# Optimization experiments

Measured on AMD Instinct MI355X. Metric: run time of the kernel, lower is better.

Reference implementation:

```python
import jax, jax.numpy as jnp
import numpy as np

B, T, IN, H, NH = 64, 512, 1024, 1024, 4
HD = H // NH  # head_dim = 256
NG = 3        # gates: z (update), r (reset), n (candidate)


def setup_inputs() -> dict:
    key = jax.random.key(0)
    k1, k2, k3, k4, k5 = jax.random.split(key, 5)
    inp = jax.random.normal(k1, (B, T, IN), dtype=jnp.float32)
    # nn.Linear(input_size, 3*hidden_size): weight [3H, IN], bias [3H]
    W = jax.random.normal(k2, (IN, NG * H), dtype=jnp.float32) / np.sqrt(IN)
    bW = jax.random.normal(k3, (NG * H,), dtype=jnp.float32) * 0.02
    # recurrent R: [num_heads, head_dim_in, num_gates, head_dim_out], std=1/sqrt(head_dim)
    R = jax.random.normal(k4, (NH, HD, NG, HD), dtype=jnp.float32) / np.sqrt(HD)
    b = jax.random.normal(k5, (NH, NG, HD), dtype=jnp.float32)
    return {"input": inp, "W": W, "bW": bW, "R": R, "b": b}


def _gru_scan(Wx, R, b, h0):
    # Wx: [T, B, NH, NG, HD], h0: [B, NH, HD]
    def step(h, wx):
        # recurrent gate preactivations: Ry[b,h,g,o] = sum_i h[b,h,i] R[h,i,g,o]
        ry = jnp.einsum('bhi,higo->bhgo', h, R)
        z = jax.nn.sigmoid(wx[:, :, 0] + ry[:, :, 0] + b[:, 0])
        r = jax.nn.sigmoid(wx[:, :, 1] + ry[:, :, 1] + b[:, 1])
        n = jnp.tanh(wx[:, :, 2] + r * ry[:, :, 2] + b[:, 2])
        h_new = z * h + (1.0 - z) * n
        return h_new, h_new

    h_last, hs = jax.lax.scan(step, h0, Wx)
    return hs, h_last  # hs: [T, B, NH, HD]


def reference(input, W, bW, R, b):
    bs, sl = input.shape[0], input.shape[1]
    # input projection for all timesteps at once
    Wx = input @ W + bW                               # [B, T, NG*H]
    Wx = Wx.reshape(bs, sl, NG, NH, HD)
    Wx = jnp.transpose(Wx, (1, 0, 3, 2, 4))           # [T, B, NH, NG, HD]
    h0 = jnp.zeros((bs, NH, HD), dtype=input.dtype)
    hs, h_last = _gru_scan(Wx, R, b, h0)
    h = jnp.transpose(hs, (1, 0, 2, 3)).reshape(bs, sl, H)   # [B, T, H]
    hn = h_last.reshape(1, bs, H)                             # [num_layers=1, B, H]
    return h, hn
```

## Files before the change

kernel.cpp:

```cpp
#include <hip/hip_runtime.h>
#include <hip/hip_fp16.h>


typedef _Float16 f16x8 __attribute__((ext_vector_type(8)));
typedef _Float16 f16x2 __attribute__((ext_vector_type(2)));
typedef float    f32x4 __attribute__((ext_vector_type(4)));

#define AS1 __attribute__((address_space(1)))
#define AS3 __attribute__((address_space(3)))

__device__ __forceinline__ void async_ld16(const void* g, void* l) {
    __builtin_amdgcn_global_load_lds((const AS1 void*)g, (AS3 void*)l, 16, 0, 0);
}

__device__ __forceinline__ float sigmoidf_(float x) {
    return 1.f / (1.f + __expf(-x));
}
__device__ __forceinline__ float tanhf_(float x) {
    float e = __expf(-2.f * fabsf(x));
    float r = (1.f - e) / (1.f + e);
    return copysignf(r, x);
}

__device__ __forceinline__ float dot2f(f16x2 a, f16x2 b, float c) {
    asm("v_dot2_f32_f16 %0, %1, %2, %0" : "+v"(c) : "v"(a), "v"(b));
    return c;
}

__global__ __launch_bounds__(256) void cast_to_f16(const float* __restrict__ in,
                                                   _Float16* __restrict__ out, int n8) {
    int i = blockIdx.x * 256 + threadIdx.x;
    if (i >= n8) return;
    const float4* p = (const float4*)in;
    float4 a = p[2 * i], b = p[2 * i + 1];
    f16x8 r;
    r[0] = (_Float16)a.x; r[1] = (_Float16)a.y; r[2] = (_Float16)a.z; r[3] = (_Float16)a.w;
    r[4] = (_Float16)b.x; r[5] = (_Float16)b.y; r[6] = (_Float16)b.z; r[7] = (_Float16)b.w;
    *(f16x8*)(out + (size_t)i * 8) = r;
}

__global__ __launch_bounds__(256) void transpose_cast(const float* __restrict__ W,
                                                      _Float16* __restrict__ WT) {
    __shared__ float tile[32][33];
    const int tx = threadIdx.x, ty = threadIdx.y;
    const int n0 = blockIdx.x * 32, k0 = blockIdx.y * 32;
#pragma unroll
    for (int j = 0; j < 32; j += 8)
        tile[ty + j][tx] = W[(size_t)(k0 + ty + j) * 3072 + n0 + tx];
    __syncthreads();
#pragma unroll
    for (int j = 0; j < 32; j += 8)
        WT[(size_t)(n0 + ty + j) * 1024 + k0 + tx] = (_Float16)tile[tx][ty + j];
}

__global__ __launch_bounds__(256) void gemm_wx(const _Float16* __restrict__ A,
                                               const _Float16* __restrict__ BT,
                                               const float* __restrict__ bW,
                                               const float* __restrict__ bR,
                                               float* __restrict__ Wx) {
    __shared__ _Float16 As[128 * 32];
    __shared__ _Float16 Bs[128 * 32];
    const int tid  = threadIdx.x;
    const int wave = tid >> 6, lane = tid & 63;
    const int m0 = blockIdx.y * 128, n0 = blockIdx.x * 128;
    const int wm = (wave >> 1) * 64, wn = (wave & 1) * 64;
    const int r16 = lane & 15, kq = lane >> 4;

    f32x4 acc[4][4];
#pragma unroll
    for (int m = 0; m < 4; m++)
#pragma unroll
        for (int n = 0; n < 4; n++) acc[m][n] = (f32x4){0.f, 0.f, 0.f, 0.f};

    const int srow = wave * 32 + (lane >> 2);
    const int scol = (lane & 3) * 8;

    for (int kt = 0; kt < 32; kt++) {
        const int k0 = kt * 32;
#pragma unroll
        for (int j = 0; j < 2; j++) {
            async_ld16(A  + (size_t)(m0 + srow + j * 16) * 1024 + k0 + scol,
                       As + (wave * 32 + j * 16) * 32);
            async_ld16(BT + (size_t)(n0 + srow + j * 16) * 1024 + k0 + scol,
                       Bs + (wave * 32 + j * 16) * 32);
        }
        __syncthreads();
        f16x8 af[4], bf[4];
#pragma unroll
        for (int m = 0; m < 4; m++) af[m] = *(const f16x8*)(As + (wm + m * 16 + r16) * 32 + kq * 8);
#pragma unroll
        for (int n = 0; n < 4; n++) bf[n] = *(const f16x8*)(Bs + (wn + n * 16 + r16) * 32 + kq * 8);
#pragma unroll
        for (int m = 0; m < 4; m++)
#pragma unroll
            for (int n = 0; n < 4; n++)
                acc[m][n] = __builtin_amdgcn_mfma_f32_16x16x32_f16(af[m], bf[n], acc[m][n], 0, 0, 0);
        __syncthreads();
    }

#pragma unroll
    for (int m = 0; m < 4; m++) {
        const int row0 = m0 + wm + m * 16 + (lane >> 4) * 4;
#pragma unroll
        for (int n = 0; n < 4; n++) {
            const int col  = n0 + wn + n * 16 + r16;
            const int g    = col >> 10, head = (col >> 8) & 3, o = col & 255;
            const float bias = bW[col] + bR[head * 768 + g * 256 + o];
#pragma unroll
            for (int q = 0; q < 4; q++) {
                const int rr = row0 + q;
                const int t = rr & 511, bb = rr >> 9;
                Wx[(((size_t)t * 64 + bb) * 12 + head * 3 + g) * 256 + o] = acc[m][n][q] + bias;
            }
        }
    }
}

__global__ __launch_bounds__(1024, 4) void scan_persist(const float* __restrict__ R,
                                                        const float* __restrict__ Wx,
                                                        float* __restrict__ out) {
    const int head = blockIdx.x >> 6;
    const int b    = blockIdx.x & 63;
    const int t    = threadIdx.x;
    const int o    = t & 255;
    const int ih   = t >> 8;

    __shared__ _Float16 h16[256];
    __shared__ float red[4][3][256];

    f16x2 Rr[3][32];
    {
        const float* Rb = R + (((size_t)head * 256 + ih * 64) * 3) * 256 + o;
#pragma unroll
        for (int i2 = 0; i2 < 32; i2++) {
#pragma unroll
            for (int g = 0; g < 3; g++) {
                const float lo = Rb[((size_t)(2 * i2) * 3 + g) * 256];
                const float hi = Rb[((size_t)(2 * i2 + 1) * 3 + g) * 256];
                f16x2 p; p[0] = (_Float16)lo; p[1] = (_Float16)hi;
                Rr[g][i2] = p;
            }
        }
    }

    float hreg = 0.f;
    float wxc0 = 0.f, wxc1 = 0.f, wxc2 = 0.f;
    if (t < 256) {
        const float* p = Wx + ((size_t)b * 12 + head * 3) * 256 + o;
        wxc0 = p[0]; wxc1 = p[256]; wxc2 = p[512];
        h16[o] = (_Float16)0.f;
    }
    __syncthreads();

    float* outp = out + (size_t)b * 512 * 1024 + head * 256 + o;

    for (int step = 0; step < 512; step++) {
        float wxn0 = 0.f, wxn1 = 0.f, wxn2 = 0.f;
        if (t < 256 && step < 511) {
            const float* p = Wx + (((size_t)(step + 1) * 64 + b) * 12 + head * 3) * 256 + o;
            wxn0 = p[0]; wxn1 = p[256]; wxn2 = p[512];
        }
        float az = 0.f, ar = 0.f, an = 0.f;
        const f16x8* hp = (const f16x8*)(h16 + ih * 64);
#pragma unroll
        for (int k = 0; k < 8; k++) {
            union { f16x8 v; f16x2 p[4]; } u;
            u.v = hp[k];
#pragma unroll
            for (int j = 0; j < 4; j++) {
                az = dot2f(Rr[0][k * 4 + j], u.p[j], az);
                ar = dot2f(Rr[1][k * 4 + j], u.p[j], ar);
                an = dot2f(Rr[2][k * 4 + j], u.p[j], an);
            }
        }
        red[ih][0][o] = az; red[ih][1][o] = ar; red[ih][2][o] = an;
        __syncthreads();
        if (t < 256) {
            const float z  = sigmoidf_(wxc0 + red[0][0][o] + red[1][0][o] + red[2][0][o] + red[3][0][o]);
            const float r  = sigmoidf_(wxc1 + red[0][1][o] + red[1][1][o] + red[2][1][o] + red[3][1][o]);
            const float n  = tanhf_(wxc2 + r * (red[0][2][o] + red[1][2][o] + red[2][2][o] + red[3][2][o]));
            const float hn = z * hreg + (1.f - z) * n;
            hreg = hn;
            outp[(size_t)step * 1024] = hn;
            h16[o] = (_Float16)hn;
        }
        wxc0 = wxn0; wxc1 = wxn1; wxc2 = wxn2;
        __syncthreads();
    }
}

__global__ __launch_bounds__(256) void copy_hn(float* __restrict__ out) {
    const int idx = blockIdx.x * 256 + threadIdx.x;
    out[(size_t)64 * 512 * 1024 + idx] =
        out[((size_t)(idx >> 10) * 512 + 511) * 1024 + (idx & 1023)];
}

extern "C" void kernel_launch(void* const* d_in, const int* in_sizes, int n_in,
                              void* d_out, int out_size, void* d_ws, size_t ws_size,
                              hipStream_t stream) {
    (void)in_sizes; (void)n_in; (void)out_size; (void)ws_size;
    const float* inp = (const float*)d_in[0];
    const float* W   = (const float*)d_in[1];
    const float* bW  = (const float*)d_in[2];
    const float* R   = (const float*)d_in[3];
    const float* bR  = (const float*)d_in[4];
    float* out = (float*)d_out;

    _Float16* A16 = (_Float16*)d_ws;
    _Float16* WT  = (_Float16*)((char*)d_ws + 67108864);
    float*    Wx  = (float*)((char*)d_ws + 73400320);

    cast_to_f16<<<16384, 256, 0, stream>>>(inp, A16, 4194304);
    transpose_cast<<<dim3(96, 32), dim3(32, 8), 0, stream>>>(W, WT);
    gemm_wx<<<dim3(24, 256), 256, 0, stream>>>(A16, WT, bW, bR, Wx);
    scan_persist<<<256, 1024, 0, stream>>>(R, Wx, out);
    copy_hn<<<256, 256, 0, stream>>>(out);
}
```

Baseline: 1.059 ms.

## Reduce GRU scan partials with lane swizzles and double-buffer the hidden state

In the scan kernel, threads are remapped so the four k-slices of one output unit sit in adjacent lanes. Their dot-product partials are then summed with two ds_swizzle butterfly steps instead of a shared-memory reduction array, which removes one __syncthreads and the LDS traffic in every one of the 512 sequential steps. The hidden state is double-buffered in padded shared memory, so reads and writes within a step do not race and one barrier per step is enough. The dot2 asm is also replaced by the compiler builtin where it is available. In exchange, the one-time R loads become less coalesced, and gate math now runs on one lane in four spread across all waves.

```diff
diff --git a/kernel.cpp b/kernel.cpp
--- a/kernel.cpp
+++ b/kernel.cpp
@@ -22,10 +22,16 @@
     return copysignf(r, x);
 }
 
+#if defined(__has_builtin) && __has_builtin(__builtin_amdgcn_fdot2)
+__device__ __forceinline__ float dot2f(f16x2 a, f16x2 b, float c) {
+    return __builtin_amdgcn_fdot2(a, b, c, false);
+}
+#else
 __device__ __forceinline__ float dot2f(f16x2 a, f16x2 b, float c) {
     asm("v_dot2_f32_f16 %0, %1, %2, %0" : "+v"(c) : "v"(a), "v"(b));
     return c;
 }
+#endif
 
 __global__ __launch_bounds__(256) void cast_to_f16(const float* __restrict__ in,
                                                    _Float16* __restrict__ out, int n8) {
@@ -122,11 +128,10 @@
     const int head = blockIdx.x >> 6;
     const int b    = blockIdx.x & 63;
     const int t    = threadIdx.x;
-    const int o    = t & 255;
-    const int ih   = t >> 8;
-
-    __shared__ _Float16 h16[256];
-    __shared__ float red[4][3][256];
+    const int o    = t >> 2;
+    const int ih   = t & 3;
+
+    __shared__ _Float16 h_s[2 * 4 * 72];
 
     f16x2 Rr[3][32];
     {
@@ -143,12 +148,13 @@
         }
     }
 
+    for (int p = t; p < 2 * 4 * 72; p += 1024) h_s[p] = (_Float16)0.f;
+
     float hreg = 0.f;
     float wxc0 = 0.f, wxc1 = 0.f, wxc2 = 0.f;
-    if (t < 256) {
+    if (ih == 0) {
         const float* p = Wx + ((size_t)b * 12 + head * 3) * 256 + o;
         wxc0 = p[0]; wxc1 = p[256]; wxc2 = p[512];
-        h16[o] = (_Float16)0.f;
     }
     __syncthreads();
 
@@ -156,12 +162,12 @@
 
     for (int step = 0; step < 512; step++) {
         float wxn0 = 0.f, wxn1 = 0.f, wxn2 = 0.f;
-        if (t < 256 && step < 511) {
+        if (ih == 0 && step < 511) {
             const float* p = Wx + (((size_t)(step + 1) * 64 + b) * 12 + head * 3) * 256 + o;
             wxn0 = p[0]; wxn1 = p[256]; wxn2 = p[512];
         }
         float az = 0.f, ar = 0.f, an = 0.f;
-        const f16x8* hp = (const f16x8*)(h16 + ih * 64);
+        const f16x8* hp = (const f16x8*)(h_s + (step & 1) * 288 + ih * 72);
 #pragma unroll
         for (int k = 0; k < 8; k++) {
             union { f16x8 v; f16x2 p[4]; } u;
@@ -173,16 +179,21 @@
                 an = dot2f(Rr[2][k * 4 + j], u.p[j], an);
             }
         }
-        red[ih][0][o] = az; red[ih][1][o] = ar; red[ih][2][o] = an;
-        __syncthreads();
-        if (t < 256) {
-            const float z  = sigmoidf_(wxc0 + red[0][0][o] + red[1][0][o] + red[2][0][o] + red[3][0][o]);
-            const float r  = sigmoidf_(wxc1 + red[0][1][o] + red[1][1][o] + red[2][1][o] + red[3][1][o]);
-            const float n  = tanhf_(wxc2 + r * (red[0][2][o] + red[1][2][o] + red[2][2][o] + red[3][2][o]));
+        az += __int_as_float(__builtin_amdgcn_ds_swizzle(__float_as_int(az), 0x041F));
+        ar += __int_as_float(__builtin_amdgcn_ds_swizzle(__float_as_int(ar), 0x041F));
+        an += __int_as_float(__builtin_amdgcn_ds_swizzle(__float_as_int(an), 0x041F));
+        az += __int_as_float(__builtin_amdgcn_ds_swizzle(__float_as_int(az), 0x081F));
+        ar += __int_as_float(__builtin_amdgcn_ds_swizzle(__float_as_int(ar), 0x081F));
+        an += __int_as_float(__builtin_amdgcn_ds_swizzle(__float_as_int(an), 0x081F));
+
+        if (ih == 0) {
+            const float z  = sigmoidf_(wxc0 + az);
+            const float r  = sigmoidf_(wxc1 + ar);
+            const float n  = tanhf_(wxc2 + r * an);
             const float hn = z * hreg + (1.f - z) * n;
             hreg = hn;
             outp[(size_t)step * 1024] = hn;
-            h16[o] = (_Float16)hn;
+            h_s[((step + 1) & 1) * 288 + (o >> 6) * 72 + (o & 63)] = (_Float16)hn;
         }
         wxc0 = wxn0; wxc1 = wxn1; wxc2 = wxn2;
         __syncthreads();
```

Result: slower. 1.246 ms (+17.7%).

## Batch GRU scan over 16 sequences per block using MFMA with register/LDS-resident R

Applied to the files above, without the earlier changes.

Replaces the per-(head,batch) dot2 scan, which used 256 blocks of 1024 threads, with an MFMA-based scan. Each of 16 blocks handles one head and 16 batch rows, so the recurrent matmul runs on matrix cores. Most of R is kept in registers and the remaining quarter in LDS. Wx is now stored in fp16, and a new repack kernel lays it out per block and timestep for vectorized loads. The trade-off is far fewer blocks on the serial critical path, extra fp16 rounding of the gate inputs, and an additional repack pass.

```diff
diff --git a/kernel.cpp b/kernel.cpp
--- a/kernel.cpp
+++ b/kernel.cpp
@@ -3,7 +3,7 @@
 
 
 typedef _Float16 f16x8 __attribute__((ext_vector_type(8)));
-typedef _Float16 f16x2 __attribute__((ext_vector_type(2)));
+typedef _Float16 f16x4 __attribute__((ext_vector_type(4)));
 typedef float    f32x4 __attribute__((ext_vector_type(4)));
 
 #define AS1 __attribute__((address_space(1)))
@@ -20,11 +20,6 @@
     float e = __expf(-2.f * fabsf(x));
     float r = (1.f - e) / (1.f + e);
     return copysignf(r, x);
-}
-
-__device__ __forceinline__ float dot2f(f16x2 a, f16x2 b, float c) {
-    asm("v_dot2_f32_f16 %0, %1, %2, %0" : "+v"(c) : "v"(a), "v"(b));
-    return c;
 }
 
 __global__ __launch_bounds__(256) void cast_to_f16(const float* __restrict__ in,
@@ -57,7 +52,7 @@
                                                const _Float16* __restrict__ BT,
                                                const float* __restrict__ bW,
                                                const float* __restrict__ bR,
-                                               float* __restrict__ Wx) {
+                                               _Float16* __restrict__ WxA) {
     __shared__ _Float16 As[128 * 32];
     __shared__ _Float16 Bs[128 * 32];
     const int tid  = threadIdx.x;
@@ -110,82 +105,150 @@
             for (int q = 0; q < 4; q++) {
                 const int rr = row0 + q;
                 const int t = rr & 511, bb = rr >> 9;
-                Wx[(((size_t)t * 64 + bb) * 12 + head * 3 + g) * 256 + o] = acc[m][n][q] + bias;
+                WxA[(((size_t)t * 64 + bb) * 12 + head * 3 + g) * 256 + o] =
+                    (_Float16)(acc[m][n][q] + bias);
             }
         }
     }
 }
 
-__global__ __launch_bounds__(1024, 4) void scan_persist(const float* __restrict__ R,
-                                                        const float* __restrict__ Wx,
-                                                        float* __restrict__ out) {
-    const int head = blockIdx.x >> 6;
-    const int b    = blockIdx.x & 63;
-    const int t    = threadIdx.x;
-    const int o    = t & 255;
-    const int ih   = t >> 8;
-
-    __shared__ _Float16 h16[256];
-    __shared__ float red[4][3][256];
-
-    f16x2 Rr[3][32];
+__global__ __launch_bounds__(256) void repack_wx(const _Float16* __restrict__ src,
+                                                 _Float16* __restrict__ dst) {
+    __shared__ _Float16 tile[16 * 768];
+    const int bx = blockIdx.x;
+    const int t = bx >> 4, head = (bx >> 2) & 3, bg = bx & 3;
+    const int tid = threadIdx.x;
     {
-        const float* Rb = R + (((size_t)head * 256 + ih * 64) * 3) * 256 + o;
-#pragma unroll
-        for (int i2 = 0; i2 < 32; i2++) {
-#pragma unroll
-            for (int g = 0; g < 3; g++) {
-                const float lo = Rb[((size_t)(2 * i2) * 3 + g) * 256];
-                const float hi = Rb[((size_t)(2 * i2 + 1) * 3 + g) * 256];
-                f16x2 p; p[0] = (_Float16)lo; p[1] = (_Float16)hi;
-                Rr[g][i2] = p;
+        const int b = tid >> 4, seg = tid & 15;
+        const _Float16* sp = src + (((size_t)t * 64 + bg * 16 + b) * 12 + head * 3) * 256 + seg * 48;
+        _Float16* tp = tile + b * 768 + seg * 48;
+#pragma unroll
+        for (int u = 0; u < 6; u++)
+            *(float4*)(tp + u * 8) = *(const float4*)(sp + u * 8);
+    }
+    __syncthreads();
+    {
+        const int o = tid;
+        _Float16 buf[48];
+#pragma unroll
+        for (int g = 0; g < 3; g++)
+#pragma unroll
+            for (int b = 0; b < 16; b++)
+                buf[g * 16 + b] = tile[b * 768 + g * 256 + o];
+        _Float16* dp = dst + (size_t)bx * 12288 + o * 48;
+#pragma unroll
+        for (int u = 0; u < 6; u++)
+            *(float4*)(dp + u * 8) = *(const float4*)(buf + u * 8);
+    }
+}
+
+__global__ __launch_bounds__(256) void scan_mfma(const float* __restrict__ R,
+                                                 const _Float16* __restrict__ Wxb,
+                                                 float* __restrict__ out) {
+    extern __shared__ char smem[];
+    _Float16* h16 = (_Float16*)smem;
+    _Float16* Rst = (_Float16*)(smem + 17024);
+
+    const int bx = blockIdx.x;
+    const int head = bx >> 2, bg = bx & 3;
+    const int tid = threadIdx.x;
+    const int w = tid >> 6, l = tid & 63;
+    const int c = l & 15, rq = l >> 4;
+
+    for (int idx = tid; idx < 3 * 64 * 256; idx += 256) {
+        const int g = idx >> 14, i = (idx >> 8) & 63, o = idx & 255;
+        Rst[((size_t)g * 256 + o) * 74 + i] =
+            (_Float16)R[(((size_t)head * 256 + 192 + i) * 3 + g) * 256 + o];
+    }
+    for (int idx = tid; idx < 2 * 16 * 266; idx += 256) h16[idx] = (_Float16)0.f;
+
+    f16x8 Bf[12][6];
+#pragma unroll
+    for (int osi = 0; osi < 4; osi++)
+#pragma unroll
+        for (int g = 0; g < 3; g++) {
+            const int o = (osi * 4 + w) * 16 + c;
+            const float* rp = R + ((size_t)head * 256 * 3 + g) * 256 + o;
+#pragma unroll
+            for (int kt = 0; kt < 6; kt++) {
+                f16x8 v;
+#pragma unroll
+                for (int j = 0; j < 8; j++)
+                    v[j] = (_Float16)rp[(size_t)(kt * 32 + rq * 8 + j) * 768];
+                Bf[osi * 3 + g][kt] = v;
             }
         }
-    }
-
-    float hreg = 0.f;
-    float wxc0 = 0.f, wxc1 = 0.f, wxc2 = 0.f;
-    if (t < 256) {
-        const float* p = Wx + ((size_t)b * 12 + head * 3) * 256 + o;
-        wxc0 = p[0]; wxc1 = p[256]; wxc2 = p[512];
-        h16[o] = (_Float16)0.f;
+
+    float hprev[4][4];
+#pragma unroll
+    for (int osi = 0; osi < 4; osi++)
+#pragma unroll
+        for (int q = 0; q < 4; q++) hprev[osi][q] = 0.f;
+
+    f16x4 wx[12];
+    {
+        const _Float16* wp = Wxb + (size_t)bx * 12288;
+#pragma unroll
+        for (int osi = 0; osi < 4; osi++)
+#pragma unroll
+            for (int g = 0; g < 3; g++)
+                wx[osi * 3 + g] = *(const f16x4*)(wp + (((osi * 4 + w) * 16 + c) * 3 + g) * 16 + rq * 4);
     }
     __syncthreads();
 
-    float* outp = out + (size_t)b * 512 * 1024 + head * 256 + o;
-
-    for (int step = 0; step < 512; step++) {
-        float wxn0 = 0.f, wxn1 = 0.f, wxn2 = 0.f;
-        if (t < 256 && step < 511) {
-            const float* p = Wx + (((size_t)(step + 1) * 64 + b) * 12 + head * 3) * 256 + o;
-            wxn0 = p[0]; wxn1 = p[256]; wxn2 = p[512];
-        }
-        float az = 0.f, ar = 0.f, an = 0.f;
-        const f16x8* hp = (const f16x8*)(h16 + ih * 64);
-#pragma unroll
-        for (int k = 0; k < 8; k++) {
-            union { f16x8 v; f16x2 p[4]; } u;
-            u.v = hp[k];
-#pragma unroll
-            for (int j = 0; j < 4; j++) {
-                az = dot2f(Rr[0][k * 4 + j], u.p[j], az);
-                ar = dot2f(Rr[1][k * 4 + j], u.p[j], ar);
-                an = dot2f(Rr[2][k * 4 + j], u.p[j], an);
+    int cur = 0;
+    for (int t = 0; t < 512; t++) {
+        const _Float16* hc = h16 + cur * (16 * 266) + c * 266 + rq * 8;
+        f32x4 acc[12];
+#pragma unroll
+        for (int n = 0; n < 12; n++) acc[n] = (f32x4){0.f, 0.f, 0.f, 0.f};
+#pragma unroll
+        for (int kt = 0; kt < 6; kt++) {
+            const f16x8 Af = *(const f16x8*)(hc + kt * 32);
+#pragma unroll
+            for (int n = 0; n < 12; n++)
+                acc[n] = __builtin_amdgcn_mfma_f32_16x16x32_f16(Af, Bf[n][kt], acc[n], 0, 0, 0);
+        }
+#pragma unroll
+        for (int kt = 6; kt < 8; kt++) {
+            const f16x8 Af = *(const f16x8*)(hc + kt * 32);
+#pragma unroll
+            for (int osi = 0; osi < 4; osi++)
+#pragma unroll
+                for (int g = 0; g < 3; g++) {
+                    const f16x8 Bs = *(const f16x8*)(Rst +
+                        ((size_t)g * 256 + (osi * 4 + w) * 16 + c) * 74 + (kt - 6) * 32 + rq * 8);
+                    acc[osi * 3 + g] =
+                        __builtin_amdgcn_mfma_f32_16x16x32_f16(Af, Bs, acc[osi * 3 + g], 0, 0, 0);
+                }
+        }
+        _Float16* hw = h16 + (cur ^ 1) * (16 * 266);
+        float* outb = out + ((size_t)(bg * 16 + rq * 4) * 512 + t) * 1024 + head * 256 + w * 16 + c;
+#pragma unroll
+        for (int osi = 0; osi < 4; osi++) {
+            const f32x4 pz = acc[osi * 3 + 0], pr = acc[osi * 3 + 1], pn = acc[osi * 3 + 2];
+            const f16x4 wz = wx[osi * 3 + 0], wr = wx[osi * 3 + 1], wn = wx[osi * 3 + 2];
+#pragma unroll
+            for (int q = 0; q < 4; q++) {
+                const float z = sigmoidf_((float)wz[q] + pz[q]);
+                const float r = sigmoidf_((float)wr[q] + pr[q]);
+                const float n = tanhf_((float)wn[q] + r * pn[q]);
+                const float h = z * hprev[osi][q] + (1.f - z) * n;
+                hprev[osi][q] = h;
+                outb[(size_t)q * 512 * 1024 + osi * 64] = h;
+                hw[(rq * 4 + q) * 266 + (osi * 4 + w) * 16 + c] = (_Float16)h;
             }
         }
-        red[ih][0][o] = az; red[ih][1][o] = ar; red[ih][2][o] = an;
+        if (t < 511) {
+            const _Float16* wp = Wxb + ((size_t)(t + 1) * 16 + bx) * 12288;
+#pragma unroll
+            for (int osi = 0; osi < 4; osi++)
+#pragma unroll
+                for (int g = 0; g < 3; g++)
+                    wx[osi * 3 + g] = *(const f16x4*)(wp + (((osi * 4 + w) * 16 + c) * 3 + g) * 16 + rq * 4);
+        }
         __syncthreads();
-        if (t < 256) {
-            const float z  = sigmoidf_(wxc0 + red[0][0][o] + red[1][0][o] + red[2][0][o] + red[3][0][o]);
-            const float r  = sigmoidf_(wxc1 + red[0][1][o] + red[1][1][o] + red[2][1][o] + red[3][1][o]);
-            const float n  = tanhf_(wxc2 + r * (red[0][2][o] + red[1][2][o] + red[2][2][o] + red[3][2][o]));
-            const float hn = z * hreg + (1.f - z) * n;
-            hreg = hn;
-            outp[(size_t)step * 1024] = hn;
-            h16[o] = (_Float16)hn;
-        }
-        wxc0 = wxn0; wxc1 = wxn1; wxc2 = wxn2;
-        __syncthreads();
+        cur ^= 1;
     }
 }
 
@@ -208,11 +271,17 @@
 
     _Float16* A16 = (_Float16*)d_ws;
     _Float16* WT  = (_Float16*)((char*)d_ws + 67108864);
-    float*    Wx  = (float*)((char*)d_ws + 73400320);
+    _Float16* WxA = (_Float16*)((char*)d_ws + 73400320);
+    _Float16* WxB = (_Float16*)((char*)d_ws + 274726912);
+
+    const int scan_lds = 17024 + 113664;
+    hipFuncSetAttribute((const void*)scan_mfma,
+                        hipFuncAttributeMaxDynamicSharedMemorySize, scan_lds);
 
     cast_to_f16<<<16384, 256, 0, stream>>>(inp, A16, 4194304);
     transpose_cast<<<dim3(96, 32), dim3(32, 8), 0, stream>>>(W, WT);
-    gemm_wx<<<dim3(24, 256), 256, 0, stream>>>(A16, WT, bW, bR, Wx);
-    scan_persist<<<256, 1024, 0, stream>>>(R, Wx, out);
+    gemm_wx<<<dim3(24, 256), 256, 0, stream>>>(A16, WT, bW, bR, WxA);
+    repack_wx<<<8192, 256, 0, stream>>>(WxA, WxB);
+    scan_mfma<<<16, 256, scan_lds, stream>>>(R, WxB, out);
     copy_hn<<<256, 256, 0, stream>>>(out);
 }
```

Result: slower. 3.519 ms (+232.4%).

## Compute recurrent GRU matvec with MFMA and register-resident R fragments

Applied to the files above, without the earlier changes.

Replaces the dot2-based scan kernel with an MFMA-based one. R is staged through LDS into per-wave register fragments, with the last k-tile read from LDS. h is broadcast as the A operand and double-buffered, removing the cross-thread LDS reduction and one barrier per step. Because the A rows are identical, most MFMA work is redundant, and register pressure is high.

```diff
diff --git a/kernel.cpp b/kernel.cpp
--- a/kernel.cpp
+++ b/kernel.cpp
@@ -3,7 +3,6 @@
 
 
 typedef _Float16 f16x8 __attribute__((ext_vector_type(8)));
-typedef _Float16 f16x2 __attribute__((ext_vector_type(2)));
 typedef float    f32x4 __attribute__((ext_vector_type(4)));
 
 #define AS1 __attribute__((address_space(1)))
@@ -20,11 +19,6 @@
     float e = __expf(-2.f * fabsf(x));
     float r = (1.f - e) / (1.f + e);
     return copysignf(r, x);
-}
-
-__device__ __forceinline__ float dot2f(f16x2 a, f16x2 b, float c) {
-    asm("v_dot2_f32_f16 %0, %1, %2, %0" : "+v"(c) : "v"(a), "v"(b));
-    return c;
 }
 
 __global__ __launch_bounds__(256) void cast_to_f16(const float* __restrict__ in,
@@ -116,76 +110,118 @@
     }
 }
 
-__global__ __launch_bounds__(1024, 4) void scan_persist(const float* __restrict__ R,
-                                                        const float* __restrict__ Wx,
-                                                        float* __restrict__ out) {
-    const int head = blockIdx.x >> 6;
-    const int b    = blockIdx.x & 63;
-    const int t    = threadIdx.x;
-    const int o    = t & 255;
-    const int ih   = t >> 8;
-
-    __shared__ _Float16 h16[256];
-    __shared__ float red[4][3][256];
-
-    f16x2 Rr[3][32];
-    {
-        const float* Rb = R + (((size_t)head * 256 + ih * 64) * 3) * 256 + o;
-#pragma unroll
-        for (int i2 = 0; i2 < 32; i2++) {
-#pragma unroll
-            for (int g = 0; g < 3; g++) {
-                const float lo = Rb[((size_t)(2 * i2) * 3 + g) * 256];
-                const float hi = Rb[((size_t)(2 * i2 + 1) * 3 + g) * 256];
-                f16x2 p; p[0] = (_Float16)lo; p[1] = (_Float16)hi;
-                Rr[g][i2] = p;
+__global__ __launch_bounds__(512) void scan_mfma(const float* __restrict__ R,
+                                                 const float* __restrict__ Wx,
+                                                 float* __restrict__ out) {
+    __shared__ _Float16 Rbuf[3 * 256 * 40];
+    __shared__ _Float16 h16[2 * 256];
+
+    const int bx = blockIdx.x;
+    const int head = bx >> 6, b = bx & 63;
+    const int t0 = threadIdx.x;
+    const int w = t0 >> 6, l = t0 & 63;
+    const int c = l & 15, kq = l >> 4;
+    const int o0 = w * 32;
+
+    f16x8 Bf[3][2][7];
+#pragma unroll
+    for (int kt = 0; kt < 8; kt++) {
+        __syncthreads();
+        for (int idx = t0; idx < 32 * 768; idx += 512) {
+            const int i2 = idx >> 8 >> 1 >> 0;
+            const int ii = idx / 768;
+            const int rem = idx - ii * 768;
+            const int g = rem >> 8, o = rem & 255;
+            Rbuf[(g * 256 + o) * 40 + ii] =
+                (_Float16)R[(((size_t)head * 256 + kt * 32 + ii) * 3 + g) * 256 + o];
+            (void)i2;
+        }
+        __syncthreads();
+        if (kt < 7) {
+#pragma unroll
+            for (int g = 0; g < 3; g++)
+#pragma unroll
+                for (int ot = 0; ot < 2; ot++)
+                    Bf[g][ot][kt] =
+                        *(const f16x8*)(Rbuf + ((size_t)(g * 256 + o0 + ot * 16 + c)) * 40 + kq * 8);
+        }
+    }
+
+    if (t0 < 512) { h16[t0] = (_Float16)0.f; }
+
+    float hprev[2] = {0.f, 0.f};
+    float wxc[3][2];
+#pragma unroll
+    for (int g = 0; g < 3; g++)
+#pragma unroll
+        for (int o2 = 0; o2 < 2; o2++)
+            wxc[g][o2] = Wx[(((size_t)0 * 64 + b) * 12 + head * 3 + g) * 256 + o0 + o2 * 16 + c];
+    __syncthreads();
+
+    float* outb = out + ((size_t)b * 512) * 1024 + head * 256;
+    int cur = 0;
+
+    for (int t = 0; t < 512; t++) {
+        f32x4 acc[3][2];
+#pragma unroll
+        for (int g = 0; g < 3; g++)
+#pragma unroll
+            for (int ot = 0; ot < 2; ot++) acc[g][ot] = (f32x4){0.f, 0.f, 0.f, 0.f};
+
+#pragma unroll
+        for (int kt = 0; kt < 7; kt++) {
+            const f16x8 Af = *(const f16x8*)(h16 + cur * 256 + kt * 32 + kq * 8);
+#pragma unroll
+            for (int g = 0; g < 3; g++)
+#pragma unroll
+                for (int ot = 0; ot < 2; ot++)
+                    acc[g][ot] = __builtin_amdgcn_mfma_f32_16x16x32_f16(Af, Bf[g][ot][kt],
+                                                                        acc[g][ot], 0, 0, 0);
+        }
+        {
+            const f16x8 Af = *(const f16x8*)(h16 + cur * 256 + 7 * 32 + kq * 8);
+#pragma unroll
+            for (int g = 0; g < 3; g++)
+#pragma unroll
+                for (int ot = 0; ot < 2; ot++) {
+                    const f16x8 Bs =
+                        *(const f16x8*)(Rbuf + ((size_t)(g * 256 + o0 + ot * 16 + c)) * 40 + kq * 8);
+                    acc[g][ot] = __builtin_amdgcn_mfma_f32_16x16x32_f16(Af, Bs,
+                                                                        acc[g][ot], 0, 0, 0);
+                }
+        }
+
+        float wxn[3][2];
+        if (t < 511) {
+#pragma unroll
+            for (int g = 0; g < 3; g++)
+#pragma unroll
+                for (int o2 = 0; o2 < 2; o2++)
+                    wxn[g][o2] = Wx[(((size_t)(t + 1) * 64 + b) * 12 + head * 3 + g) * 256 +
+                                    o0 + o2 * 16 + c];
+        } else {
+            wxn[0][0] = wxn[0][1] = wxn[1][0] = wxn[1][1] = wxn[2][0] = wxn[2][1] = 0.f;
+        }
+
+#pragma unroll
+        for (int o2 = 0; o2 < 2; o2++) {
+            const float z = sigmoidf_(wxc[0][o2] + acc[0][o2][0]);
+            const float r = sigmoidf_(wxc[1][o2] + acc[1][o2][0]);
+            const float n = tanhf_(wxc[2][o2] + r * acc[2][o2][0]);
+            const float h = z * hprev[o2] + (1.f - z) * n;
+            hprev[o2] = h;
+            if (kq == 0) {
+                outb[(size_t)t * 1024 + o0 + o2 * 16 + c] = h;
+                h16[(cur ^ 1) * 256 + o0 + o2 * 16 + c] = (_Float16)h;
             }
         }
-    }
-
-    float hreg = 0.f;
-    float wxc0 = 0.f, wxc1 = 0.f, wxc2 = 0.f;
-    if (t < 256) {
-        const float* p = Wx + ((size_t)b * 12 + head * 3) * 256 + o;
-        wxc0 = p[0]; wxc1 = p[256]; wxc2 = p[512];
-        h16[o] = (_Float16)0.f;
-    }
-    __syncthreads();
-
-    float* outp = out + (size_t)b * 512 * 1024 + head * 256 + o;
-
-    for (int step = 0; step < 512; step++) {
-        float wxn0 = 0.f, wxn1 = 0.f, wxn2 = 0.f;
-        if (t < 256 && step < 511) {
-            const float* p = Wx + (((size_t)(step + 1) * 64 + b) * 12 + head * 3) * 256 + o;
-            wxn0 = p[0]; wxn1 = p[256]; wxn2 = p[512];
-        }
-        float az = 0.f, ar = 0.f, an = 0.f;
-        const f16x8* hp = (const f16x8*)(h16 + ih * 64);
-#pragma unroll
-        for (int k = 0; k < 8; k++) {
-            union { f16x8 v; f16x2 p[4]; } u;
-            u.v = hp[k];
-#pragma unroll
-            for (int j = 0; j < 4; j++) {
-                az = dot2f(Rr[0][k * 4 + j], u.p[j], az);
-                ar = dot2f(Rr[1][k * 4 + j], u.p[j], ar);
-                an = dot2f(Rr[2][k * 4 + j], u.p[j], an);
-            }
-        }
-        red[ih][0][o] = az; red[ih][1][o] = ar; red[ih][2][o] = an;
-        __syncthreads();
-        if (t < 256) {
-            const float z  = sigmoidf_(wxc0 + red[0][0][o] + red[1][0][o] + red[2][0][o] + red[3][0][o]);
-            const float r  = sigmoidf_(wxc1 + red[0][1][o] + red[1][1][o] + red[2][1][o] + red[3][1][o]);
-            const float n  = tanhf_(wxc2 + r * (red[0][2][o] + red[1][2][o] + red[2][2][o] + red[3][2][o]));
-            const float hn = z * hreg + (1.f - z) * n;
-            hreg = hn;
-            outp[(size_t)step * 1024] = hn;
-            h16[o] = (_Float16)hn;
-        }
-        wxc0 = wxn0; wxc1 = wxn1; wxc2 = wxn2;
-        __syncthreads();
+#pragma unroll
+        for (int g = 0; g < 3; g++)
+#pragma unroll
+            for (int o2 = 0; o2 < 2; o2++) wxc[g][o2] = wxn[g][o2];
+
+        __syncthreads();
+        cur ^= 1;
     }
 }
 
@@ -213,6 +249,6 @@
     cast_to_f16<<<16384, 256, 0, stream>>>(inp, A16, 4194304);
     transpose_cast<<<dim3(96, 32), dim3(32, 8), 0, stream>>>(W, WT);
     gemm_wx<<<dim3(24, 256), 256, 0, stream>>>(A16, WT, bW, bR, Wx);
-    scan_persist<<<256, 1024, 0, stream>>>(R, Wx, out);
+    scan_mfma<<<256, 512, 0, stream>>>(R, Wx, out);
     copy_hn<<<256, 256, 0, stream>>>(out);
 }
```

New measurement: 1.057 ms. Within noise of the previous version (-0.2%).
